# Performance work log

Measured on AMD Instinct MI355X. Metric: run time of the kernel, lower is better.

## Reference

```python
import jax, jax.numpy as jnp
import numpy as np

B, C, T = 8, 64, 128

def _conv(x, w, b, stride=1, pad=1, groups=1):
    y = jax.lax.conv_general_dilated(x, w, (stride, stride), [(pad, pad), (pad, pad)],
                                     feature_group_count=groups,
                                     dimension_numbers=('NCHW', 'OIHW', 'NCHW'))
    return y + b[None, :, None, None]

def _lrelu(x):
    return jnp.where(x > 0, x, 0.1 * x)

def _ps4(A, Bt, Ct, Dt):
    # qiancha(A,B,C,D) interleaves channels with stride 4; PixelShuffle(2) then maps
    # group index j in [0..3] to pixel offset (j//2, j%2): A->(0,0), B->(0,1), C->(1,0), D->(1,1)
    b, c, h, w = A.shape
    s = jnp.stack([A, Bt, Ct, Dt], axis=2).reshape(b, c, 2, 2, h, w)
    return s.transpose(0, 1, 4, 2, 5, 3).reshape(b, c, 2 * h, 2 * w)

def _il2(A, Bt):
    # qiancha2: stride-2 channel interleave
    b, c, h, w = A.shape
    return jnp.stack([A, Bt], axis=2).reshape(b, 2 * c, h, w)

def setup_inputs():
    key = jax.random.key(0)
    ks = jax.random.split(key, 20)
    def w(k, shape):
        return 0.05 * jax.random.normal(k, shape, dtype=jnp.float32)
    d = {}
    d['x'] = jax.random.normal(ks[0], (B, C, T, T), dtype=jnp.float32)
    d['w_hwc'] = w(ks[1], (3 * C, C, 1, 1)); d['b_hwc'] = w(ks[2], (3 * C,))
    d['w_dw'] = w(ks[3], (3 * C, 1, 3, 3)); d['b_dw'] = w(ks[4], (3 * C,))
    d['w_hw'] = w(ks[5], (C, C, 3, 3)); d['b_hw'] = w(ks[6], (C,))
    d['w_cw'] = w(ks[7], (T, T, 3, 3)); d['b_cw'] = w(ks[8], (T,))
    d['w_hc'] = w(ks[9], (T, T, 3, 3)); d['b_hc'] = w(ks[10], (T,))
    d['w_down'] = w(ks[11], (C, 2 * C, 2, 2)); d['b_down'] = w(ks[12], (C,))
    d['w_l1'] = w(ks[13], (C, C, 3, 3)); d['b_l1'] = w(ks[14], (C,))
    d['w_l2'] = w(ks[15], (C, C, 3, 3)); d['b_l2'] = w(ks[16], (C,))
    return d

def reference(x, w_hwc, b_hwc, w_dw, b_dw, w_hw, b_hw, w_cw, b_cw, w_hc, b_hc,
              w_down, b_down, w_l1, b_l1, w_l2, b_l2):
    c = x.shape[1]
    # 1x1 expand then depthwise 3x3 -> three gating maps
    hwc = _conv(_conv(x, w_hwc, b_hwc, pad=0), w_dw, b_dw, pad=1, groups=3 * c)
    HW, CW, HC = jnp.split(hwc, 3, axis=1)
    x_hw = _lrelu(_conv(x, w_hw, b_hw)) * HW
    x_cw = _lrelu(_conv(x.transpose(0, 2, 1, 3), w_cw, b_cw)).transpose(0, 2, 1, 3) * CW
    x_hc = _lrelu(_conv(x.transpose(0, 3, 2, 1), w_hc, b_hc)).transpose(0, 3, 2, 1) * HC
    xqc1 = _ps4(x, x_hw, x_cw, x_hc)
    xqc2 = _ps4(x_hc, x_cw, x_hw, x)
    xqc = _il2(xqc1, xqc2)                              # [B, 2C, 2T, 2T]
    out = _conv(xqc, w_down, b_down, stride=2, pad=0) + x
    out1 = _lrelu(_conv(out, w_l1, b_l1))
    out1 = _lrelu(_conv(out1, w_l2, b_l2))
    return x + out1
```

## Files before the change

kernel.cpp:

```cpp
#include <hip/hip_runtime.h>
#include <hip/hip_bf16.h>

#define BB 8
#define CC 64
#define TT 128
#define PP (TT*TT)
#define C3 192

typedef __hip_bfloat16 bf16;
typedef __attribute__((ext_vector_type(8))) short short8;
typedef __attribute__((ext_vector_type(4))) float floatx4;

__device__ __forceinline__ float b2f(bf16 v){ return __bfloat162float(v); }
__device__ __forceinline__ bf16 f2b(float v){ return __float2bfloat16(v); }
__device__ __forceinline__ short8 lds8(const bf16* p){ return *(const short8*)(const void*)p; }

__global__ void k_wpk(const float* __restrict__ w_down, const float* __restrict__ w_hc,
                      const float* __restrict__ w_cw,  const float* __restrict__ w_hwc,
                      const float* __restrict__ w_hw,  const float* __restrict__ w_l1,
                      const float* __restrict__ w_l2,  const float* __restrict__ w_dw,
                      const float* __restrict__ b_hwc, const float* __restrict__ b_dw,
                      bf16* __restrict__ wpkd,
                      bf16* __restrict__ wpkhw, bf16* __restrict__ wpkl1,
                      bf16* __restrict__ wpkl2, bf16* __restrict__ wpkcw,
                      bf16* __restrict__ wpkhc, bf16* __restrict__ wpkg,
                      float* __restrict__ bg){
  int i = blockIdx.x*256 + threadIdx.x;
  if (i < 147456){
    int j = i & 7, lane = (i>>3) & 63, mm = (i>>9) & 7, kk = (i>>12) & 3, t = i >> 14;
    int m = mm*16 + (lane & 15);
    int k = kk*32 + (lane>>4)*8 + j;
    wpkcw[i] = f2b(w_cw[m*1152 + k*9 + t]);
    wpkhc[i] = f2b(w_hc[m*1152 + k*9 + t]);
  }
  if (i < 36864){
    int j = i & 7, lane = (i>>3) & 63, mm = (i>>9) & 3, kk = (i>>11) & 1, t = i >> 12;
    int oc = mm*16 + (lane & 15);
    int ic = kk*32 + (lane>>4)*8 + j;
    int s = oc*576 + ic*9 + t;
    wpkhw[i] = f2b(w_hw[s]);
    wpkl1[i] = f2b(w_l1[s]);
    wpkl2[i] = f2b(w_l2[s]);
  }
  if (i < 110592){
    int j = i & 7, lane = (i>>3) & 63, rest = i >> 9;
    int mm = rest % 12, tk = rest / 12;
    int oc = mm*16 + (lane & 15);
    int ic = (tk & 1)*32 + (lane>>4)*8 + j;
    int t = tk >> 1;
    wpkg[i] = f2b(w_dw[oc*9 + t] * w_hwc[oc*64 + ic]);
  }
  if (i < 1728){
    int cls = i / C3, oc = i % C3;
    int ch = cls / 3, cw = cls % 3;
    float S = 0.f;
    for (int dh = (ch==0?1:0); dh <= (ch==2?1:2); ++dh)
      for (int dw = (cw==0?1:0); dw <= (cw==2?1:2); ++dw)
        S += w_dw[oc*9 + dh*3 + dw];
    bg[cls*C3 + oc] = b_dw[oc] + b_hwc[oc]*S;
  }
  if (i < 16384){
    int j = i & 7, lane = (i>>3) & 63, mm = (i>>9) & 3, kk = i >> 11;
    int m = mm*16 + (lane & 15);
    int k = kk*32 + (lane>>4)*8 + j;
    int s = k >> 6, c = k & 63;
    wpkd[i] = f2b(w_down[m*512 + c*8 + s] + w_down[m*512 + c*8 + 7 - s]);
  }
}

__global__ void k_pack(const float* __restrict__ x, bf16* __restrict__ xh,
                       bf16* __restrict__ xb16){
  int h = blockIdx.x, b = blockIdx.y;
  __shared__ float xs[64][129];
  for (int idx = threadIdx.x; idx < 2048; idx += 256){
    int c = idx >> 5, w4 = (idx & 31)*4;
    float4 v = *(const float4*)(x + ((size_t)b*CC + c)*PP + h*TT + w4);
    bf16 o4[4] = { f2b(v.x), f2b(v.y), f2b(v.z), f2b(v.w) };
    *(uint2*)(xb16 + ((size_t)b*CC + c)*PP + h*TT + w4) = *(uint2*)o4;
    xs[c][w4] = v.x; xs[c][w4+1] = v.y; xs[c][w4+2] = v.z; xs[c][w4+3] = v.w;
  }
  __syncthreads();
  for (int idx = threadIdx.x; idx < 8192; idx += 256){
    int w = idx >> 6, c = idx & 63;
    xh[(((size_t)b*TT + h)*TT + w)*64 + c] = f2b(xs[c][w]);
  }
}

__global__ void k_xw(const float* __restrict__ x, bf16* __restrict__ xW){
  int c = blockIdx.x, b = blockIdx.y;
  __shared__ float xs2[32][129];
  const float* src = x + ((size_t)b*CC + c)*PP;
  bf16* dst = xW + ((size_t)b*CC + c)*PP;
  for (int s = 0; s < 4; ++s){
    for (int idx = threadIdx.x; idx < 4096; idx += 256){
      int hl = idx >> 7, w = idx & 127;
      xs2[hl][w] = src[(s*32 + hl)*TT + w];
    }
    __syncthreads();
    for (int idx = threadIdx.x; idx < 4096; idx += 256){
      int w = idx >> 5, hl = idx & 31;
      dst[w*TT + s*32 + hl] = f2b(xs2[hl][w]);
    }
    __syncthreads();
  }
}

__global__ __launch_bounds__(256)
void k_ghwm(const bf16* __restrict__ xh, const bf16* __restrict__ wpkg,
            const bf16* __restrict__ wpkhw, const float* __restrict__ bg,
            const float* __restrict__ b_hw, bf16* __restrict__ xhwh,
            bf16* __restrict__ g){
  int w0b = blockIdx.x*64, h = blockIdx.y, b = blockIdx.z;
  int tid = threadIdx.x, lane = tid & 63, wv = tid >> 6;
  int nlo = lane & 15, quad = lane >> 4;
  __shared__ bf16 xs[3][66][64];
  for (int idx = tid; idx < 1584; idx += 256){
    int dh = idx / 528, r = idx % 528, wi = r >> 3, ch = r & 7;
    int gh = h + dh - 1, gw = w0b + wi - 1;
    uint4 v = make_uint4(0,0,0,0);
    if (gh >= 0 && gh < TT && gw >= 0 && gw < TT)
      v = *(const uint4*)(xh + (((size_t)b*TT + gh)*TT + gw)*64 + ch*8);
    *(uint4*)(&xs[dh][wi][((ch ^ (wi & 7)))*8]) = v;
  }
  __syncthreads();
  floatx4 acc[4][4] = {};
  #pragma unroll
  for (int t = 0; t < 9; ++t){
    int dh = t/3, dw = t%3;
    int swk = (nlo + dw) & 7;
    #pragma unroll
    for (int kk = 0; kk < 2; ++kk){
      int pc = ((kk*4 + quad) ^ swk)*8;
      short8 bfv[4];
      #pragma unroll
      for (int nn = 0; nn < 4; ++nn)
        bfv[nn] = lds8(&xs[dh][nn*16 + nlo + dw][pc]);
      short8 a0 = *(const short8*)(const void*)(wpkhw + (((t*2+kk)*4  + wv   )*64 + lane)*8);
      short8 a1 = *(const short8*)(const void*)(wpkg  + (((t*2+kk)*12 + wv   )*64 + lane)*8);
      short8 a2 = *(const short8*)(const void*)(wpkg  + (((t*2+kk)*12 + 4+wv )*64 + lane)*8);
      short8 a3 = *(const short8*)(const void*)(wpkg  + (((t*2+kk)*12 + 8+wv )*64 + lane)*8);
      #pragma unroll
      for (int nn = 0; nn < 4; ++nn){
        acc[0][nn] = __builtin_amdgcn_mfma_f32_16x16x32_bf16(a0, bfv[nn], acc[0][nn], 0,0,0);
        acc[1][nn] = __builtin_amdgcn_mfma_f32_16x16x32_bf16(a1, bfv[nn], acc[1][nn], 0,0,0);
        acc[2][nn] = __builtin_amdgcn_mfma_f32_16x16x32_bf16(a2, bfv[nn], acc[2][nn], 0,0,0);
        acc[3][nn] = __builtin_amdgcn_mfma_f32_16x16x32_bf16(a3, bfv[nn], acc[3][nn], 0,0,0);
      }
    }
  }
  int ch_cls3 = ((h == 0) ? 0 : (h == TT-1) ? 2 : 1)*3;
  int oc0 = wv*16 + quad*4;
  float4 bhw = *(const float4*)(b_hw + oc0);
  #pragma unroll
  for (int nn = 0; nn < 4; ++nn){
    int w = w0b + nn*16 + nlo;
    int cw_cls = (w == 0) ? 0 : (w == TT-1) ? 2 : 1;
    const float* bgrow = bg + (ch_cls3 + cw_cls)*C3;
    float4 bg0 = *(const float4*)(bgrow + oc0);
    float bga[4] = { bg0.x, bg0.y, bg0.z, bg0.w };
    float bha[4] = { bhw.x, bhw.y, bhw.z, bhw.w };
    bf16 o4[4];
    #pragma unroll
    for (int r = 0; r < 4; ++r){
      float hv = acc[0][nn][r] + bha[r];
      hv = hv > 0.f ? hv : 0.1f*hv;
      float gv = b2f(f2b(acc[1][nn][r] + bga[r]));
      o4[r] = f2b(hv * gv);
    }
    *(uint2*)(xhwh + (((size_t)b*PP + h*TT + w))*64 + oc0) = *(uint2*)o4;
  }
  __syncthreads();
  bf16* tb = &xs[0][0][0];
  #pragma unroll
  for (int p = 0; p < 2; ++p){
    #pragma unroll
    for (int nn = 0; nn < 4; ++nn){
      int wl = nn*16 + nlo;
      int w = w0b + wl;
      int cw_cls = (w == 0) ? 0 : (w == TT-1) ? 2 : 1;
      float4 bgp = *(const float4*)(bg + (ch_cls3 + cw_cls)*C3 + 64 + p*64 + oc0);
      float bga[4] = { bgp.x, bgp.y, bgp.z, bgp.w };
      #pragma unroll
      for (int r = 0; r < 4; ++r)
        tb[(p*64 + oc0 + r)*72 + wl] = f2b(acc[2+p][nn][r] + bga[r]);
    }
  }
  __syncthreads();
  #pragma unroll
  for (int i = 0; i < 4; ++i){
    int idx = i*256 + tid;
    int row = idx >> 3, wc = (idx & 7)*8;
    uint4 v = *(const uint4*)(tb + row*72 + wc);
    *(uint4*)(g + ((size_t)b*C3 + 64 + row)*PP + h*TT + w0b + wc) = v;
  }
}

__global__ __launch_bounds__(256)
void k_c3x3m(const bf16* __restrict__ in, const bf16* __restrict__ wpk,
             const float* __restrict__ bias,
             const float* __restrict__ resx, bf16* __restrict__ yb,
             float* __restrict__ yf, int mode){
  int h = blockIdx.x, b = blockIdx.y;
  int tid = threadIdx.x, lane = tid & 63, wv = tid >> 6;
  int nlo = lane & 15, quad = lane >> 4;
  __shared__ bf16 xs[3][130][64];
  for (int idx = tid; idx < 3120; idx += 256){
    int dh = idx / 1040, r = idx % 1040, wi = r >> 3, ch = r & 7;
    int gh = h + dh - 1, gw = wi - 1;
    uint4 v = make_uint4(0,0,0,0);
    if (gh >= 0 && gh < TT && gw >= 0 && gw < TT)
      v = *(const uint4*)(in + (((size_t)b*TT + gh)*TT + gw)*64 + ch*8);
    *(uint4*)(&xs[dh][wi][((ch ^ (wi & 7)))*8]) = v;
  }
  __syncthreads();
  floatx4 acc[8] = {};
  #pragma unroll
  for (int t = 0; t < 9; ++t){
    int dh = t/3, dw = t%3;
    int swk = (nlo + dw) & 7;
    #pragma unroll
    for (int kk = 0; kk < 2; ++kk){
      short8 a = *(const short8*)(const void*)(wpk + (((t*2+kk)*4+wv)*64 + lane)*8);
      int pc = ((kk*4 + quad) ^ swk)*8;
      #pragma unroll
      for (int nn = 0; nn < 8; ++nn){
        short8 bf = lds8(&xs[dh][nn*16 + nlo + dw][pc]);
        acc[nn] = __builtin_amdgcn_mfma_f32_16x16x32_bf16(a, bf, acc[nn], 0,0,0);
      }
    }
  }
  int oc0 = wv*16 + quad*4;
  float4 bs = *(const float4*)(bias + oc0);
  float bsa[4] = { bs.x, bs.y, bs.z, bs.w };
  #pragma unroll
  for (int nn = 0; nn < 8; ++nn){
    int w = nn*16 + nlo;
    int pi = h*TT + w;
    if (mode == 1){
      bf16 o4[4];
      #pragma unroll
      for (int r = 0; r < 4; ++r){
        float v = acc[nn][r] + bsa[r];
        o4[r] = f2b(v > 0.f ? v : 0.1f*v);
      }
      *(uint2*)(yb + ((size_t)b*PP + pi)*64 + oc0) = *(uint2*)o4;
    } else {
      #pragma unroll
      for (int r = 0; r < 4; ++r){
        int oc = oc0 + r;
        float v = acc[nn][r] + bsa[r];
        v = v > 0.f ? v : 0.1f*v;
        yf[((size_t)b*CC + oc)*PP + pi] = v + resx[((size_t)b*CC + oc)*PP + pi];
      }
    }
  }
}

__global__ __launch_bounds__(256)
void k_cwm(const bf16* __restrict__ xW, const bf16* __restrict__ wpkcw,
           const float* __restrict__ bias, const bf16* __restrict__ g,
           bf16* __restrict__ xcw){
  int w0b = blockIdx.x*64, c = blockIdx.y, b = blockIdx.z;
  int tid = threadIdx.x, lane = tid & 63, wv = tid >> 6;
  int nlo = lane & 15, quad = lane >> 4;
  __shared__ bf16 xs[66][128];
  floatx4 acc[2][4] = {};
  for (int dc = 0; dc < 3; ++dc){
    int cc = c + dc - 1;
    if (cc < 0 || cc >= CC) continue;
    __syncthreads();
    for (int idx = tid; idx < 1056; idx += 256){
      int s = idx >> 4, ch = idx & 15;
      int gw = w0b - 1 + s;
      uint4 v = make_uint4(0,0,0,0);
      if (gw >= 0 && gw < TT)
        v = *(const uint4*)(xW + (((size_t)b*CC + cc)*TT + gw)*TT + ch*8);
      *(uint4*)(&xs[s][((ch ^ (s & 7)))*8]) = v;
    }
    __syncthreads();
    #pragma unroll
    for (int dw = 0; dw < 3; ++dw){
      int t = dc*3 + dw;
      int swk = (nlo + dw) & 7;
      #pragma unroll
      for (int kk = 0; kk < 4; ++kk){
        short8 a0 = *(const short8*)(const void*)(wpkcw + (((t*4+kk)*8 + wv*2    )*64 + lane)*8);
        short8 a1 = *(const short8*)(const void*)(wpkcw + (((t*4+kk)*8 + wv*2 + 1)*64 + lane)*8);
        int pc = ((kk*4 + quad) ^ swk)*8;
        #pragma unroll
        for (int nn = 0; nn < 4; ++nn){
          short8 bf = lds8(&xs[nn*16 + nlo + dw][pc]);
          acc[0][nn] = __builtin_amdgcn_mfma_f32_16x16x32_bf16(a0, bf, acc[0][nn], 0,0,0);
          acc[1][nn] = __builtin_amdgcn_mfma_f32_16x16x32_bf16(a1, bf, acc[1][nn], 0,0,0);
        }
      }
    }
  }
  #pragma unroll
  for (int ml = 0; ml < 2; ++ml){
    int ho0 = (wv*2 + ml)*16 + quad*4;
    float4 bs = *(const float4*)(bias + ho0);
    float bsa[4] = { bs.x, bs.y, bs.z, bs.w };
    #pragma unroll
    for (int nn = 0; nn < 4; ++nn){
      int w = w0b + nn*16 + nlo;
      #pragma unroll
      for (int r = 0; r < 4; ++r){
        int ho = ho0 + r;
        float v = acc[ml][nn][r] + bsa[r];
        v = v > 0.f ? v : 0.1f*v;
        v *= b2f(g[((size_t)b*C3 + 64 + c)*PP + ho*TT + w]);
        xcw[((size_t)b*CC + c)*PP + ho*TT + w] = f2b(v);
      }
    }
  }
}

__global__ __launch_bounds__(256)
void k_hcm(const bf16* __restrict__ xb16, const bf16* __restrict__ wpkhc,
           const float* __restrict__ bias, const bf16* __restrict__ g,
           bf16* __restrict__ xhch){
  int h = blockIdx.x, b = blockIdx.y;
  int tid = threadIdx.x, lane = tid & 63, wv = tid >> 6;
  int nlo = lane & 15, quad = lane >> 4;
  __shared__ bf16 xs[66][128];
  floatx4 acc[2][4] = {};
  for (int dh = 0; dh < 3; ++dh){
    int gh = h + dh - 1;
    __syncthreads();
    for (int idx = tid; idx < 1056; idx += 256){
      int s = idx >> 4, ch = idx & 15;
      int cc = s - 1;
      uint4 v = make_uint4(0,0,0,0);
      if (cc >= 0 && cc < CC && gh >= 0 && gh < TT)
        v = *(const uint4*)(xb16 + (((size_t)b*CC + cc)*TT + gh)*TT + ch*8);
      *(uint4*)(&xs[s][((ch ^ (s & 7)))*8]) = v;
    }
    __syncthreads();
    #pragma unroll
    for (int dc = 0; dc < 3; ++dc){
      int t = dh*3 + dc;
      int swk = (nlo + dc) & 7;
      #pragma unroll
      for (int kk = 0; kk < 4; ++kk){
        short8 a0 = *(const short8*)(const void*)(wpkhc + (((t*4+kk)*8 + wv*2    )*64 + lane)*8);
        short8 a1 = *(const short8*)(const void*)(wpkhc + (((t*4+kk)*8 + wv*2 + 1)*64 + lane)*8);
        int pc = ((kk*4 + quad) ^ swk)*8;
        #pragma unroll
        for (int nn = 0; nn < 4; ++nn){
          short8 bf = lds8(&xs[nn*16 + nlo + dc][pc]);
          acc[0][nn] = __builtin_amdgcn_mfma_f32_16x16x32_bf16(a0, bf, acc[0][nn], 0,0,0);
          acc[1][nn] = __builtin_amdgcn_mfma_f32_16x16x32_bf16(a1, bf, acc[1][nn], 0,0,0);
        }
      }
    }
  }
  #pragma unroll
  for (int ml = 0; ml < 2; ++ml){
    int wo0 = (wv*2 + ml)*16 + quad*4;
    float4 bs = *(const float4*)(bias + wo0);
    float bsa[4] = { bs.x, bs.y, bs.z, bs.w };
    #pragma unroll
    for (int nn = 0; nn < 4; ++nn){
      int c = nn*16 + nlo;
      bf16 gg[4];
      *(uint2*)gg = *(const uint2*)(g + ((size_t)b*C3 + 128 + c)*PP + h*TT + wo0);
      #pragma unroll
      for (int r = 0; r < 4; ++r){
        float v = acc[ml][nn][r] + bsa[r];
        v = v > 0.f ? v : 0.1f*v;
        xhch[((size_t)b*PP + h*TT + wo0 + r)*64 + c] = f2b(v * b2f(gg[r]));
      }
    }
  }
}

__global__ __launch_bounds__(256)
void k_downm(const bf16* __restrict__ xh, const bf16* __restrict__ xhwh,
             const bf16* __restrict__ xcwn, const bf16* __restrict__ xhch,
             const bf16* __restrict__ wpkd, const float* __restrict__ x,
             const float* __restrict__ bias, bf16* __restrict__ outh){
  int h = blockIdx.x, b = blockIdx.y;
  int tid = threadIdx.x, lane = tid & 63, wv = tid >> 6;
  int nlo = lane & 15, quad = lane >> 4;
  int p0 = h*TT;
  __shared__ bf16 xs[128][76];
  for (int idx = tid; idx < 1024; idx += 256){
    int c = idx >> 4, w8 = (idx & 15)*8;
    bf16 tmp[8];
    *(uint4*)tmp = *(const uint4*)(xcwn + ((size_t)b*CC + c)*PP + p0 + w8);
    #pragma unroll
    for (int j = 0; j < 8; ++j) xs[w8+j][c] = tmp[j];
  }
  __syncthreads();
  int n0 = wv*32;
  floatx4 acc[4][2] = {};
  #pragma unroll
  for (int kk = 0; kk < 8; ++kk){
    int s = kk >> 1;
    int ko = (kk & 1)*32 + quad*8;
    short8 bfr[2];
    #pragma unroll
    for (int nn = 0; nn < 2; ++nn){
      int p = n0 + nn*16 + nlo;
      if (s == 2){
        bfr[nn] = lds8(&xs[p][ko]);
      } else {
        const bf16* src = (s == 0) ? xh : (s == 1) ? xhwh : xhch;
        bfr[nn] = *(const short8*)(const void*)(src + ((size_t)b*PP + p0 + p)*64 + ko);
      }
    }
    #pragma unroll
    for (int mm = 0; mm < 4; ++mm){
      short8 a = *(const short8*)(const void*)(wpkd + ((kk*4+mm)*64 + lane)*8);
      acc[mm][0] = __builtin_amdgcn_mfma_f32_16x16x32_bf16(a, bfr[0], acc[mm][0], 0,0,0);
      acc[mm][1] = __builtin_amdgcn_mfma_f32_16x16x32_bf16(a, bfr[1], acc[mm][1], 0,0,0);
    }
  }
  #pragma unroll
  for (int mm = 0; mm < 4; ++mm){
    int o0 = mm*16 + quad*4;
    float4 bs = *(const float4*)(bias + o0);
    float bsa[4] = { bs.x, bs.y, bs.z, bs.w };
    #pragma unroll
    for (int nn = 0; nn < 2; ++nn){
      int p = n0 + nn*16 + nlo;
      bf16 o4[4];
      #pragma unroll
      for (int r = 0; r < 4; ++r){
        float v = acc[mm][nn][r] + bsa[r] + x[((size_t)b*CC + o0 + r)*PP + p0 + p];
        o4[r] = f2b(v);
      }
      *(uint2*)(outh + ((size_t)b*PP + p0 + p)*64 + o0) = *(uint2*)o4;
    }
  }
}

extern "C" void kernel_launch(void* const* d_in, const int* in_sizes, int n_in,
                              void* d_out, int out_size, void* d_ws, size_t ws_size,
                              hipStream_t stream) {
  const float* x      = (const float*)d_in[0];
  const float* w_hwc  = (const float*)d_in[1];
  const float* b_hwc  = (const float*)d_in[2];
  const float* w_dw   = (const float*)d_in[3];
  const float* b_dw   = (const float*)d_in[4];
  const float* w_hw   = (const float*)d_in[5];
  const float* b_hw   = (const float*)d_in[6];
  const float* w_cw   = (const float*)d_in[7];
  const float* b_cw   = (const float*)d_in[8];
  const float* w_hc   = (const float*)d_in[9];
  const float* b_hc   = (const float*)d_in[10];
  const float* w_down = (const float*)d_in[11];
  const float* b_down = (const float*)d_in[12];
  const float* w_l1   = (const float*)d_in[13];
  const float* b_l1   = (const float*)d_in[14];
  const float* w_l2   = (const float*)d_in[15];
  const float* b_l2   = (const float*)d_in[16];
  float* out = (float*)d_out;

  char* ws = (char*)d_ws;
  bf16*  wpkd  = (bf16*) (ws + 0);
  float* bg    = (float*)(ws + 36864);
  bf16*  wpkhw = (bf16*) (ws + 65536);
  bf16*  wpkl1 = (bf16*) (ws + 139264);
  bf16*  wpkl2 = (bf16*) (ws + 212992);
  bf16*  wpkcw = (bf16*) (ws + 294912);
  bf16*  wpkhc = (bf16*) (ws + 589824);
  bf16*  wpkg  = (bf16*) (ws + 884736);

  k_wpk<<<576, 256, 0, stream>>>(w_down, w_hc, w_cw, w_hwc, w_hw, w_l1, w_l2,
                                 w_dw, b_hwc, b_dw,
                                 wpkd, wpkhw, wpkl1, wpkl2, wpkcw, wpkhc,
                                 wpkg, bg);

  if (ws_size >= 153092096ull) {
    bf16* g    = (bf16*)(ws + 2097152);
    bf16* xh   = (bf16*)(ws + 52428800);
    bf16* xW   = (bf16*)(ws + 69206016);
    bf16* xb16 = (bf16*)(ws + 85983232);
    bf16* xhwh = (bf16*)(ws + 102760448);
    bf16* xcw  = (bf16*)(ws + 119537664);
    bf16* xhch = (bf16*)(ws + 136314880);
    bf16* outh = xW;
    bf16* o1h  = xb16;

    k_pack<<<dim3(TT, BB), 256, 0, stream>>>(x, xh, xb16);
    k_xw<<<dim3(CC, BB), 256, 0, stream>>>(x, xW);
    k_ghwm<<<dim3(2, TT, BB), 256, 0, stream>>>(xh, wpkg, wpkhw, bg, b_hw, xhwh, g);
    k_cwm  <<<dim3(2, CC, BB), 256, 0, stream>>>(xW, wpkcw, b_cw, g, xcw);
    k_hcm  <<<dim3(TT, BB), 256, 0, stream>>>(xb16, wpkhc, b_hc, g, xhch);
    k_downm<<<dim3(TT, BB), 256, 0, stream>>>(xh, xhwh, xcw, xhch, wpkd, x, b_down, outh);
    k_c3x3m<<<dim3(TT, BB), 256, 0, stream>>>(outh, wpkl1, b_l1, nullptr, o1h, nullptr, 1);
    k_c3x3m<<<dim3(TT, BB), 256, 0, stream>>>(o1h, wpkl2, b_l2, x, nullptr, out, 2);
  } else {
    char* P = ws + 2097152;
    bf16* g_b    = (bf16*)(P);
    bf16* xh_b   = (bf16*)(P + 6291456);
    bf16* xW_b   = (bf16*)(P + 8388608);
    bf16* xb_b   = (bf16*)(P + 10485760);
    bf16* xhwh_b = (bf16*)(P + 12582912);
    bf16* xcw_b  = (bf16*)(P + 14680064);
    bf16* xhch_b = (bf16*)(P + 16777216);
    bf16* outh_b = xW_b;
    bf16* o1h_b  = xb_b;
    for (int b = 0; b < BB; ++b){
      const float* xb = x + (size_t)b*CC*PP;
      float* outb = out + (size_t)b*CC*PP;
      k_pack<<<dim3(TT, 1), 256, 0, stream>>>(xb, xh_b, xb_b);
      k_xw<<<dim3(CC, 1), 256, 0, stream>>>(xb, xW_b);
      k_ghwm<<<dim3(2, TT, 1), 256, 0, stream>>>(xh_b, wpkg, wpkhw, bg, b_hw, xhwh_b, g_b);
      k_cwm  <<<dim3(2, CC, 1), 256, 0, stream>>>(xW_b, wpkcw, b_cw, g_b, xcw_b);
      k_hcm  <<<dim3(TT, 1), 256, 0, stream>>>(xb_b, wpkhc, b_hc, g_b, xhch_b);
      k_downm<<<dim3(TT, 1), 256, 0, stream>>>(xh_b, xhwh_b, xcw_b, xhch_b, wpkd, xb, b_down, outh_b);
      k_c3x3m<<<dim3(TT, 1), 256, 0, stream>>>(outh_b, wpkl1, b_l1, nullptr, o1h_b, nullptr, 1);
      k_c3x3m<<<dim3(TT, 1), 256, 0, stream>>>(o1h_b, wpkl2, b_l2, xb, nullptr, outb, 2);
    }
  }
}
```

Before: 326.3 us.

## Widen k_ghwm tile to full row and transpose xW from bf16 copy

k_ghwm now processes a full 128-wide row per block instead of two 64-wide halves. The doubled accumulator count amortizes weight loads and halo staging over more MFMAs, with launch bounds hinting two blocks per CU. k_xw now reads the already-converted bf16 tensor with 16-byte loads instead of fp32 scalars, which cuts global read traffic and drops one barrier per stage. The costs are a larger LDS footprint, higher register pressure from the 4x8 accumulator tile, and half as many blocks for k_ghwm.

New measurement: 304.8 us. 1.07x faster.

```diff
diff --git a/kernel.cpp b/kernel.cpp
--- a/kernel.cpp
+++ b/kernel.cpp
@@ -86,44 +86,47 @@
   }
 }
 
-__global__ void k_xw(const float* __restrict__ x, bf16* __restrict__ xW){
+__global__ void k_xw(const bf16* __restrict__ xb16, bf16* __restrict__ xW){
   int c = blockIdx.x, b = blockIdx.y;
-  __shared__ float xs2[32][129];
-  const float* src = x + ((size_t)b*CC + c)*PP;
-  bf16* dst = xW + ((size_t)b*CC + c)*PP;
+  __shared__ unsigned short xs2[32][140];
+  const bf16* src = xb16 + ((size_t)b*CC + c)*PP;
+  unsigned short* dst = (unsigned short*)(xW + ((size_t)b*CC + c)*PP);
   for (int s = 0; s < 4; ++s){
-    for (int idx = threadIdx.x; idx < 4096; idx += 256){
-      int hl = idx >> 7, w = idx & 127;
-      xs2[hl][w] = src[(s*32 + hl)*TT + w];
+    if (s) __syncthreads();
+    for (int idx = threadIdx.x; idx < 512; idx += 256){
+      int hl = idx >> 4, w8 = (idx & 15)*8;
+      unsigned short tmp[8];
+      *(uint4*)tmp = *(const uint4*)(src + (s*32 + hl)*TT + w8);
+      #pragma unroll
+      for (int j = 0; j < 8; ++j) xs2[hl][w8+j] = tmp[j];
     }
     __syncthreads();
     for (int idx = threadIdx.x; idx < 4096; idx += 256){
       int w = idx >> 5, hl = idx & 31;
-      dst[w*TT + s*32 + hl] = f2b(xs2[hl][w]);
-    }
-    __syncthreads();
-  }
-}
-
-__global__ __launch_bounds__(256)
+      dst[w*TT + s*32 + hl] = xs2[hl][w];
+    }
+  }
+}
+
+__global__ __launch_bounds__(256, 2)
 void k_ghwm(const bf16* __restrict__ xh, const bf16* __restrict__ wpkg,
             const bf16* __restrict__ wpkhw, const float* __restrict__ bg,
             const float* __restrict__ b_hw, bf16* __restrict__ xhwh,
             bf16* __restrict__ g){
-  int w0b = blockIdx.x*64, h = blockIdx.y, b = blockIdx.z;
+  int h = blockIdx.x, b = blockIdx.y;
   int tid = threadIdx.x, lane = tid & 63, wv = tid >> 6;
   int nlo = lane & 15, quad = lane >> 4;
-  __shared__ bf16 xs[3][66][64];
-  for (int idx = tid; idx < 1584; idx += 256){
-    int dh = idx / 528, r = idx % 528, wi = r >> 3, ch = r & 7;
-    int gh = h + dh - 1, gw = w0b + wi - 1;
+  __shared__ bf16 xs[3][130][64];
+  for (int idx = tid; idx < 3120; idx += 256){
+    int dh = idx / 1040, r = idx % 1040, wi = r >> 3, ch = r & 7;
+    int gh = h + dh - 1, gw = wi - 1;
     uint4 v = make_uint4(0,0,0,0);
     if (gh >= 0 && gh < TT && gw >= 0 && gw < TT)
       v = *(const uint4*)(xh + (((size_t)b*TT + gh)*TT + gw)*64 + ch*8);
     *(uint4*)(&xs[dh][wi][((ch ^ (wi & 7)))*8]) = v;
   }
   __syncthreads();
-  floatx4 acc[4][4] = {};
+  floatx4 acc[4][8] = {};
   #pragma unroll
   for (int t = 0; t < 9; ++t){
     int dh = t/3, dw = t%3;
@@ -131,20 +134,17 @@
     #pragma unroll
     for (int kk = 0; kk < 2; ++kk){
       int pc = ((kk*4 + quad) ^ swk)*8;
-      short8 bfv[4];
-      #pragma unroll
-      for (int nn = 0; nn < 4; ++nn)
-        bfv[nn] = lds8(&xs[dh][nn*16 + nlo + dw][pc]);
       short8 a0 = *(const short8*)(const void*)(wpkhw + (((t*2+kk)*4  + wv   )*64 + lane)*8);
       short8 a1 = *(const short8*)(const void*)(wpkg  + (((t*2+kk)*12 + wv   )*64 + lane)*8);
       short8 a2 = *(const short8*)(const void*)(wpkg  + (((t*2+kk)*12 + 4+wv )*64 + lane)*8);
       short8 a3 = *(const short8*)(const void*)(wpkg  + (((t*2+kk)*12 + 8+wv )*64 + lane)*8);
       #pragma unroll
-      for (int nn = 0; nn < 4; ++nn){
-        acc[0][nn] = __builtin_amdgcn_mfma_f32_16x16x32_bf16(a0, bfv[nn], acc[0][nn], 0,0,0);
-        acc[1][nn] = __builtin_amdgcn_mfma_f32_16x16x32_bf16(a1, bfv[nn], acc[1][nn], 0,0,0);
-        acc[2][nn] = __builtin_amdgcn_mfma_f32_16x16x32_bf16(a2, bfv[nn], acc[2][nn], 0,0,0);
-        acc[3][nn] = __builtin_amdgcn_mfma_f32_16x16x32_bf16(a3, bfv[nn], acc[3][nn], 0,0,0);
+      for (int nn = 0; nn < 8; ++nn){
+        short8 bfv = lds8(&xs[dh][nn*16 + nlo + dw][pc]);
+        acc[0][nn] = __builtin_amdgcn_mfma_f32_16x16x32_bf16(a0, bfv, acc[0][nn], 0,0,0);
+        acc[1][nn] = __builtin_amdgcn_mfma_f32_16x16x32_bf16(a1, bfv, acc[1][nn], 0,0,0);
+        acc[2][nn] = __builtin_amdgcn_mfma_f32_16x16x32_bf16(a2, bfv, acc[2][nn], 0,0,0);
+        acc[3][nn] = __builtin_amdgcn_mfma_f32_16x16x32_bf16(a3, bfv, acc[3][nn], 0,0,0);
       }
     }
   }
@@ -152,11 +152,10 @@
   int oc0 = wv*16 + quad*4;
   float4 bhw = *(const float4*)(b_hw + oc0);
   #pragma unroll
-  for (int nn = 0; nn < 4; ++nn){
-    int w = w0b + nn*16 + nlo;
+  for (int nn = 0; nn < 8; ++nn){
+    int w = nn*16 + nlo;
     int cw_cls = (w == 0) ? 0 : (w == TT-1) ? 2 : 1;
-    const float* bgrow = bg + (ch_cls3 + cw_cls)*C3;
-    float4 bg0 = *(const float4*)(bgrow + oc0);
+    float4 bg0 = *(const float4*)(bg + (ch_cls3 + cw_cls)*C3 + oc0);
     float bga[4] = { bg0.x, bg0.y, bg0.z, bg0.w };
     float bha[4] = { bhw.x, bhw.y, bhw.z, bhw.w };
     bf16 o4[4];
@@ -174,24 +173,23 @@
   #pragma unroll
   for (int p = 0; p < 2; ++p){
     #pragma unroll
-    for (int nn = 0; nn < 4; ++nn){
+    for (int nn = 0; nn < 8; ++nn){
       int wl = nn*16 + nlo;
-      int w = w0b + wl;
-      int cw_cls = (w == 0) ? 0 : (w == TT-1) ? 2 : 1;
+      int cw_cls = (wl == 0) ? 0 : (wl == TT-1) ? 2 : 1;
       float4 bgp = *(const float4*)(bg + (ch_cls3 + cw_cls)*C3 + 64 + p*64 + oc0);
       float bga[4] = { bgp.x, bgp.y, bgp.z, bgp.w };
       #pragma unroll
       for (int r = 0; r < 4; ++r)
-        tb[(p*64 + oc0 + r)*72 + wl] = f2b(acc[2+p][nn][r] + bga[r]);
+        tb[(p*64 + oc0 + r)*132 + wl] = f2b(acc[2+p][nn][r] + bga[r]);
     }
   }
   __syncthreads();
   #pragma unroll
-  for (int i = 0; i < 4; ++i){
+  for (int i = 0; i < 8; ++i){
     int idx = i*256 + tid;
-    int row = idx >> 3, wc = (idx & 7)*8;
-    uint4 v = *(const uint4*)(tb + row*72 + wc);
-    *(uint4*)(g + ((size_t)b*C3 + 64 + row)*PP + h*TT + w0b + wc) = v;
+    int row = idx >> 4, wc = (idx & 15)*8;
+    uint4 v = *(const uint4*)(tb + row*132 + wc);
+    *(uint4*)(g + ((size_t)b*C3 + 64 + row)*PP + h*TT + wc) = v;
   }
 }
 
@@ -485,8 +483,8 @@
     bf16* o1h  = xb16;
 
     k_pack<<<dim3(TT, BB), 256, 0, stream>>>(x, xh, xb16);
-    k_xw<<<dim3(CC, BB), 256, 0, stream>>>(x, xW);
-    k_ghwm<<<dim3(2, TT, BB), 256, 0, stream>>>(xh, wpkg, wpkhw, bg, b_hw, xhwh, g);
+    k_xw<<<dim3(CC, BB), 256, 0, stream>>>(xb16, xW);
+    k_ghwm<<<dim3(TT, BB), 256, 0, stream>>>(xh, wpkg, wpkhw, bg, b_hw, xhwh, g);
     k_cwm  <<<dim3(2, CC, BB), 256, 0, stream>>>(xW, wpkcw, b_cw, g, xcw);
     k_hcm  <<<dim3(TT, BB), 256, 0, stream>>>(xb16, wpkhc, b_hc, g, xhch);
     k_downm<<<dim3(TT, BB), 256, 0, stream>>>(xh, xhwh, xcw, xhch, wpkd, x, b_down, outh);
@@ -507,8 +505,8 @@
       const float* xb = x + (size_t)b*CC*PP;
       float* outb = out + (size_t)b*CC*PP;
       k_pack<<<dim3(TT, 1), 256, 0, stream>>>(xb, xh_b, xb_b);
-      k_xw<<<dim3(CC, 1), 256, 0, stream>>>(xb, xW_b);
-      k_ghwm<<<dim3(2, TT, 1), 256, 0, stream>>>(xh_b, wpkg, wpkhw, bg, b_hw, xhwh_b, g_b);
+      k_xw<<<dim3(CC, 1), 256, 0, stream>>>(xb_b, xW_b);
+      k_ghwm<<<dim3(TT, 1), 256, 0, stream>>>(xh_b, wpkg, wpkhw, bg, b_hw, xhwh_b, g_b);
       k_cwm  <<<dim3(2, CC, 1), 256, 0, stream>>>(xW_b, wpkcw, b_cw, g_b, xcw_b);
       k_hcm  <<<dim3(TT, 1), 256, 0, stream>>>(xb_b, wpkhc, b_hc, g_b, xhch_b);
       k_downm<<<dim3(TT, 1), 256, 0, stream>>>(xh_b, xhwh_b, xcw_b, xhch_b, wpkd, xb, b_down, outh_b);
```
